# Performance work log

Hardware: AMD Instinct MI355X
Metric: run time of the kernel (lower is better)

Reference implementation:

```python
import jax, jax.numpy as jnp
import numpy as np

NUM_BINS = 31  # default num_bins in SummaryStats.from_array
N = 64 * 1024 * 1024  # 64M elements, 256 MB fp32 -> memory-bound reductions


def setup_inputs() -> dict:
    key = jax.random.key(0)
    x = jax.random.normal(key, (N,), dtype=jnp.float32)
    return {"x": x}


def reference(x):
    # SummaryStats.from_sharded_array on a single device (spec is fully replicated,
    # so _single_shard_histogram_array semantics apply: last bin is right-inclusive,
    # which matches jnp.histogram / searchsorted binning).
    x = x.ravel()
    mn = x.min()
    mx = x.max()
    nonzero_count = jnp.count_nonzero(x)
    num = jnp.asarray(x.size, dtype=nonzero_count.dtype)
    s = x.sum()
    ss = (x ** 2).sum()

    # histogram_bin_edges on stack([min, max]) with bins=NUM_BINS -> linspace(min, max, NUM_BINS+1)
    edges = jnp.linspace(mn, mx, NUM_BINS + 1)
    # bin index: values in [edges[i], edges[i+1]), last bin inclusive of edges[-1].
    idx = jnp.clip(jnp.searchsorted(edges, x, side="right") - 1, 0, NUM_BINS - 1)
    # exclude values strictly outside [min, max] (none here, but faithful to the compare logic)
    valid = (x >= edges[0]) & (x <= edges[-1])
    counts = jnp.zeros((NUM_BINS,), dtype=jnp.int32).at[idx].add(
        valid.astype(jnp.int32)
    )
    return mn, mx, num, nonzero_count, s, ss, counts, edges
```

## Files before the change

### kernel.cpp

```cpp
#include <hip/hip_runtime.h>

#define NBINS 31
#define NB1 2048
#define NB2 2048
#define HPITCH 128
#define NREP 8
#define GSTRIDE 32

struct Partial {
    unsigned int mnk, mxk, nz, pad;
    double s, ss;
};
#define OFF_G (NB1 * 32)
#define OFF_CTR (OFF_G + NBINS * NREP * GSTRIDE * 4)

__device__ __forceinline__ unsigned int fkey(float f) {
    unsigned int u = __float_as_uint(f);
    return (u & 0x80000000u) ? ~u : (u | 0x80000000u);
}
__device__ __forceinline__ float funkey(unsigned int k) {
    return (k & 0x80000000u) ? __uint_as_float(k & 0x7FFFFFFFu)
                             : __uint_as_float(~k);
}
__device__ __forceinline__ float edge_at(float mn, float step, float fi) {
    return __fadd_rn(mn, __fmul_rn(fi, step));
}

__device__ __forceinline__ void acc4(float4 v, float& mn, float& mx, float& s, float& ss,
                                     unsigned int& nz) {
    mn = fminf(mn, fminf(fminf(v.x, v.y), fminf(v.z, v.w)));
    mx = fmaxf(mx, fmaxf(fmaxf(v.x, v.y), fmaxf(v.z, v.w)));
    s  += (v.x + v.y) + (v.z + v.w);
    ss += (v.x * v.x + v.y * v.y) + (v.z * v.z + v.w * v.w);
    nz += (v.x != 0.f) + (v.y != 0.f) + (v.z != 0.f) + (v.w != 0.f);
}

__global__ void __launch_bounds__(256) k_reduce(const float* __restrict__ x, long long n,
                                                Partial* __restrict__ part,
                                                unsigned int* __restrict__ ghist,
                                                unsigned int* __restrict__ ctr) {
    if (blockIdx.x == 0) {
        if (threadIdx.x < NBINS * NREP) ghist[threadIdx.x * GSTRIDE] = 0u;
        if (threadIdx.x == 255) *ctr = 0u;
    }

    long long n4 = n >> 2;
    const float4* __restrict__ x4 = (const float4*)x;
    float mn = INFINITY, mx = -INFINITY, s = 0.f, ss = 0.f;
    unsigned int nz = 0u;

    long long stride = (long long)gridDim.x * blockDim.x;
    long long i = (long long)blockIdx.x * blockDim.x + threadIdx.x;
    for (; i + 3 * stride < n4; i += 4 * stride) {
        float4 a = x4[i], b = x4[i + stride], c = x4[i + 2 * stride], d = x4[i + 3 * stride];
        acc4(a, mn, mx, s, ss, nz);
        acc4(b, mn, mx, s, ss, nz);
        acc4(c, mn, mx, s, ss, nz);
        acc4(d, mn, mx, s, ss, nz);
    }
    for (; i < n4; i += stride) acc4(x4[i], mn, mx, s, ss, nz);
    if (blockIdx.x == 0 && threadIdx.x < (int)(n & 3)) {
        float v = x[(n4 << 2) + threadIdx.x];
        mn = fminf(mn, v); mx = fmaxf(mx, v);
        s += v; ss += v * v; nz += (v != 0.f);
    }

    double sd = (double)s, ssd = (double)ss;
    #pragma unroll
    for (int off = 32; off > 0; off >>= 1) {
        mn = fminf(mn, __shfl_down(mn, off));
        mx = fmaxf(mx, __shfl_down(mx, off));
        sd  += __shfl_down(sd, off);
        ssd += __shfl_down(ssd, off);
        nz  += __shfl_down(nz, off);
    }
    __shared__ float lmn[4], lmx[4];
    __shared__ double lsum[4], lss[4];
    __shared__ unsigned int lnz[4];
    int w = threadIdx.x >> 6;
    if ((threadIdx.x & 63) == 0) { lmn[w] = mn; lmx[w] = mx; lsum[w] = sd; lss[w] = ssd; lnz[w] = nz; }
    __syncthreads();
    if (threadIdx.x == 0) {
        Partial p;
        p.mnk = fkey(fminf(fminf(lmn[0], lmn[1]), fminf(lmn[2], lmn[3])));
        p.mxk = fkey(fmaxf(fmaxf(lmx[0], lmx[1]), fmaxf(lmx[2], lmx[3])));
        p.nz  = lnz[0] + lnz[1] + lnz[2] + lnz[3];
        p.pad = 0;
        p.s  = lsum[0] + lsum[1] + lsum[2] + lsum[3];
        p.ss = lss[0] + lss[1] + lss[2] + lss[3];
        part[blockIdx.x] = p;
    }
}

__device__ __forceinline__ void bump(float v, float mn, float step, float inv,
                                     unsigned int* __restrict__ hist, int slot) {
    int b = (int)((v - mn) * inv);
    b = b > 30 ? 30 : b;
    float bf = (float)b;
    float lo = edge_at(mn, step, bf);
    float hi = edge_at(mn, step, bf + 1.0f);
    b += (v >= hi);
    b -= (v < lo);
    b = b > 30 ? 30 : b;
    atomicAdd(&hist[(b << 7) + slot], 1u);
}

__global__ void __launch_bounds__(256) k_hist(const float* __restrict__ x, long long n,
                                              const Partial* __restrict__ part,
                                              unsigned int* __restrict__ ghist,
                                              unsigned int* __restrict__ ctr,
                                              float* __restrict__ out) {
    __shared__ unsigned int hist[NBINS * HPITCH];
    __shared__ unsigned int lmnk[4], lmxk[4];
    __shared__ int islast;
    int tid = threadIdx.x;
    for (int j = tid; j < NBINS * HPITCH; j += 256) hist[j] = 0u;

    unsigned int mnk = 0xFFFFFFFFu, mxk = 0u;
    for (int ii = tid; ii < NB1; ii += 256) {
        uint2 p = *(const uint2*)&part[ii].mnk;
        mnk = min(mnk, p.x); mxk = max(mxk, p.y);
    }
    #pragma unroll
    for (int off = 32; off > 0; off >>= 1) {
        mnk = min(mnk, __shfl_down(mnk, off));
        mxk = max(mxk, __shfl_down(mxk, off));
    }
    int w = tid >> 6;
    if ((tid & 63) == 0) { lmnk[w] = mnk; lmxk[w] = mxk; }
    __syncthreads();
    float mn = funkey(min(min(lmnk[0], lmnk[1]), min(lmnk[2], lmnk[3])));
    float mx = funkey(max(max(lmxk[0], lmxk[1]), max(lmxk[2], lmxk[3])));
    float step = (mx - mn) / 31.0f;
    float inv  = 31.0f / (mx - mn);

    if (blockIdx.x == 0) {
        unsigned long long nz = 0ull; double s = 0.0, ss = 0.0;
        for (int ii = tid; ii < NB1; ii += 256) {
            Partial p = part[ii];
            nz += p.nz; s += p.s; ss += p.ss;
        }
        #pragma unroll
        for (int off = 32; off > 0; off >>= 1) {
            nz += __shfl_down(nz, off);
            s  += __shfl_down(s, off);
            ss += __shfl_down(ss, off);
        }
        __shared__ unsigned long long lnz[4];
        __shared__ double ls[4], lss2[4];
        if ((tid & 63) == 0) { lnz[w] = nz; ls[w] = s; lss2[w] = ss; }
        __syncthreads();
        if (tid == 0) {
            out[0] = mn;
            out[1] = mx;
            out[2] = (float)n;
            out[3] = (float)(lnz[0] + lnz[1] + lnz[2] + lnz[3]);
            out[4] = (float)(ls[0] + ls[1] + ls[2] + ls[3]);
            out[5] = (float)(lss2[0] + lss2[1] + lss2[2] + lss2[3]);
        }
        if (tid < NBINS + 1)
            out[6 + NBINS + tid] = (tid == NBINS) ? mx : edge_at(mn, step, (float)tid);
    }

    int slot = tid & (HPITCH - 1);
    long long n4 = n >> 2;
    const float4* __restrict__ x4 = (const float4*)x;
    long long stride = (long long)gridDim.x * blockDim.x;
    long long i = (long long)blockIdx.x * blockDim.x + tid;
    for (; i + stride < n4; i += 2 * stride) {
        float4 a = x4[i], b = x4[i + stride];
        bump(a.x, mn, step, inv, hist, slot); bump(a.y, mn, step, inv, hist, slot);
        bump(a.z, mn, step, inv, hist, slot); bump(a.w, mn, step, inv, hist, slot);
        bump(b.x, mn, step, inv, hist, slot); bump(b.y, mn, step, inv, hist, slot);
        bump(b.z, mn, step, inv, hist, slot); bump(b.w, mn, step, inv, hist, slot);
    }
    for (; i < n4; i += stride) {
        float4 a = x4[i];
        bump(a.x, mn, step, inv, hist, slot); bump(a.y, mn, step, inv, hist, slot);
        bump(a.z, mn, step, inv, hist, slot); bump(a.w, mn, step, inv, hist, slot);
    }
    if (blockIdx.x == 0 && tid < (int)(n & 3))
        bump(x[(n4 << 2) + tid], mn, step, inv, hist, slot);
    __syncthreads();

    int lane = tid & 63;
    int rep = blockIdx.x & (NREP - 1);
    for (int b = w; b < NBINS; b += 4) {
        const unsigned int* row = &hist[b << 7];
        uint2 q = *(const uint2*)(row + (lane << 1));
        unsigned int sv = q.x + q.y;
        #pragma unroll
        for (int off = 32; off > 0; off >>= 1) sv += __shfl_down(sv, off);
        if (lane == 0 && sv) atomicAdd(&ghist[(b * NREP + rep) * GSTRIDE], sv);
    }

    __syncthreads();
    if (tid == 0) {
        __threadfence();
        islast = (atomicAdd(ctr, 1u) == (unsigned int)(gridDim.x - 1));
    }
    __syncthreads();
    if (islast && tid < NBINS) {
        unsigned int tot = 0;
        #pragma unroll
        for (int r = 0; r < NREP; ++r)
            tot += atomicAdd(&ghist[(tid * NREP + r) * GSTRIDE], 0u);
        out[6 + tid] = (float)tot;
    }
}

extern "C" void kernel_launch(void* const* d_in, const int* in_sizes, int n_in,
                              void* d_out, int out_size, void* d_ws, size_t ws_size,
                              hipStream_t stream) {
    const float* x = (const float*)d_in[0];
    long long n = (long long)in_sizes[0];
    char* ws = (char*)d_ws;
    Partial* part = (Partial*)ws;
    unsigned int* ghist = (unsigned int*)(ws + OFF_G);
    unsigned int* ctr = (unsigned int*)(ws + OFF_CTR);
    float* out = (float*)d_out;

    k_reduce<<<dim3(NB1), dim3(256), 0, stream>>>(x, n, part, ghist, ctr);
    k_hist<<<dim3(NB2), dim3(256), 0, stream>>>(x, n, part, ghist, ctr, out);
}
```

Measured before the change: 463.8 us.

## Reverse histogram pass order to reuse cache and move final sum to kernel

The histogram pass now walks its grid-stride range from the end back to the start. The reduce pass reads the array forward, so the tail of the array, which it touched last, may still be resident in the large last-level cache when the second pass begins. The last-block atomic counter and its fences are replaced by a small third kernel that sums the replicated global bins. This adds one kernel launch but removes the per-block counter atomic and threadfence.

Result: faster. 408.3 us (-12.0%).

```diff
diff --git a/kernel.cpp b/kernel.cpp
--- a/kernel.cpp
+++ b/kernel.cpp
@@ -12,7 +12,6 @@
     double s, ss;
 };
 #define OFF_G (NB1 * 32)
-#define OFF_CTR (OFF_G + NBINS * NREP * GSTRIDE * 4)
 
 __device__ __forceinline__ unsigned int fkey(float f) {
     unsigned int u = __float_as_uint(f);
@@ -37,12 +36,8 @@
 
 __global__ void __launch_bounds__(256) k_reduce(const float* __restrict__ x, long long n,
                                                 Partial* __restrict__ part,
-                                                unsigned int* __restrict__ ghist,
-                                                unsigned int* __restrict__ ctr) {
-    if (blockIdx.x == 0) {
-        if (threadIdx.x < NBINS * NREP) ghist[threadIdx.x * GSTRIDE] = 0u;
-        if (threadIdx.x == 255) *ctr = 0u;
-    }
+                                                unsigned int* __restrict__ ghist) {
+    if (blockIdx.x == 0 && threadIdx.x < NBINS * NREP) ghist[threadIdx.x * GSTRIDE] = 0u;
 
     long long n4 = n >> 2;
     const float4* __restrict__ x4 = (const float4*)x;
@@ -108,11 +103,9 @@
 __global__ void __launch_bounds__(256) k_hist(const float* __restrict__ x, long long n,
                                               const Partial* __restrict__ part,
                                               unsigned int* __restrict__ ghist,
-                                              unsigned int* __restrict__ ctr,
                                               float* __restrict__ out) {
     __shared__ unsigned int hist[NBINS * HPITCH];
     __shared__ unsigned int lmnk[4], lmxk[4];
-    __shared__ int islast;
     int tid = threadIdx.x;
     for (int j = tid; j < NBINS * HPITCH; j += 256) hist[j] = 0u;
 
@@ -166,21 +159,26 @@
     long long n4 = n >> 2;
     const float4* __restrict__ x4 = (const float4*)x;
     long long stride = (long long)gridDim.x * blockDim.x;
-    long long i = (long long)blockIdx.x * blockDim.x + tid;
-    for (; i + stride < n4; i += 2 * stride) {
-        float4 a = x4[i], b = x4[i + stride];
-        bump(a.x, mn, step, inv, hist, slot); bump(a.y, mn, step, inv, hist, slot);
-        bump(a.z, mn, step, inv, hist, slot); bump(a.w, mn, step, inv, hist, slot);
-        bump(b.x, mn, step, inv, hist, slot); bump(b.y, mn, step, inv, hist, slot);
-        bump(b.z, mn, step, inv, hist, slot); bump(b.w, mn, step, inv, hist, slot);
-    }
-    for (; i < n4; i += stride) {
+    long long base = (long long)blockIdx.x * blockDim.x + tid;
+
+    if (blockIdx.x == 0 && tid < (int)(n & 3))
+        bump(x[(n4 << 2) + tid], mn, step, inv, hist, slot);
+
+    long long nsteps = (n4 - base + stride - 1) / (2 * stride);
+    if (nsteps < 0) nsteps = 0;
+    for (long long i = base + 2 * nsteps * stride; i < n4; i += stride) {
         float4 a = x4[i];
         bump(a.x, mn, step, inv, hist, slot); bump(a.y, mn, step, inv, hist, slot);
         bump(a.z, mn, step, inv, hist, slot); bump(a.w, mn, step, inv, hist, slot);
     }
-    if (blockIdx.x == 0 && tid < (int)(n & 3))
-        bump(x[(n4 << 2) + tid], mn, step, inv, hist, slot);
+    for (long long k = nsteps - 1; k >= 0; --k) {
+        long long i = base + 2 * k * stride;
+        float4 b = x4[i + stride], a = x4[i];
+        bump(b.x, mn, step, inv, hist, slot); bump(b.y, mn, step, inv, hist, slot);
+        bump(b.z, mn, step, inv, hist, slot); bump(b.w, mn, step, inv, hist, slot);
+        bump(a.x, mn, step, inv, hist, slot); bump(a.y, mn, step, inv, hist, slot);
+        bump(a.z, mn, step, inv, hist, slot); bump(a.w, mn, step, inv, hist, slot);
+    }
     __syncthreads();
 
     int lane = tid & 63;
@@ -193,19 +191,17 @@
         for (int off = 32; off > 0; off >>= 1) sv += __shfl_down(sv, off);
         if (lane == 0 && sv) atomicAdd(&ghist[(b * NREP + rep) * GSTRIDE], sv);
     }
-
-    __syncthreads();
-    if (tid == 0) {
-        __threadfence();
-        islast = (atomicAdd(ctr, 1u) == (unsigned int)(gridDim.x - 1));
-    }
-    __syncthreads();
-    if (islast && tid < NBINS) {
+}
+
+__global__ void __launch_bounds__(64) k_final(const unsigned int* __restrict__ ghist,
+                                              float* __restrict__ out) {
+    int t = threadIdx.x;
+    if (t < NBINS) {
         unsigned int tot = 0;
         #pragma unroll
         for (int r = 0; r < NREP; ++r)
-            tot += atomicAdd(&ghist[(tid * NREP + r) * GSTRIDE], 0u);
-        out[6 + tid] = (float)tot;
+            tot += ghist[(t * NREP + r) * GSTRIDE];
+        out[6 + t] = (float)tot;
     }
 }
 
@@ -217,9 +213,9 @@
     char* ws = (char*)d_ws;
     Partial* part = (Partial*)ws;
     unsigned int* ghist = (unsigned int*)(ws + OFF_G);
-    unsigned int* ctr = (unsigned int*)(ws + OFF_CTR);
     float* out = (float*)d_out;
 
-    k_reduce<<<dim3(NB1), dim3(256), 0, stream>>>(x, n, part, ghist, ctr);
-    k_hist<<<dim3(NB2), dim3(256), 0, stream>>>(x, n, part, ghist, ctr, out);
-}
+    k_reduce<<<dim3(NB1), dim3(256), 0, stream>>>(x, n, part, ghist);
+    k_hist<<<dim3(NB2), dim3(256), 0, stream>>>(x, n, part, ghist, out);
+    k_final<<<dim3(1), dim3(64), 0, stream>>>(ghist, out);
+}
```
